# Performance work log

Hardware: AMD Instinct MI355X
Metric: run time of the kernel (lower is better)

## Reference

```python
import jax, jax.numpy as jnp
import numpy as np

B, N, DIM_IN, DIM_OUT, EMBED, CHEB_K = 32, 2000, 64, 64, 16, 3


def setup_inputs() -> dict:
    key = jax.random.key(0)
    ks = jax.random.split(key, 6)
    return {
        "x": jax.random.normal(ks[0], (B, N, DIM_IN), dtype=jnp.float32),
        "node_embeddings": jax.random.normal(ks[1], (N, EMBED), dtype=jnp.float32),
        "nodevec1": jax.random.normal(ks[2], (N, EMBED), dtype=jnp.float32),
        "nodevec2": jax.random.normal(ks[3], (EMBED, N), dtype=jnp.float32),
        "weights_pool": jax.random.normal(ks[4], (EMBED, CHEB_K, DIM_IN, DIM_OUT), dtype=jnp.float32) * 0.1,
        "bias_pool": jax.random.normal(ks[5], (EMBED, DIM_OUT), dtype=jnp.float32) * 0.1,
    }


def reference(x, node_embeddings, nodevec1, nodevec2, weights_pool, bias_pool):
    n = node_embeddings.shape[0]
    # adaptive adjacency: softmax(relu(nodevec1 @ nodevec2)) over rows' neighbors
    s = jax.nn.softmax(jax.nn.relu(nodevec1 @ nodevec2), axis=1)  # [N, N]
    # Chebyshev polynomial stack: T0 = I, T1 = S, Tk = 2 S Tk-1 - Tk-2
    support_set = [jnp.eye(n, dtype=x.dtype), s]
    for _ in range(2, CHEB_K):
        support_set.append(2.0 * s @ support_set[-1] - support_set[-2])
    supports = jnp.stack(support_set, axis=0)  # [K, N, N]
    # node-conditioned weights / bias
    weights = jnp.einsum('nd,dkio->nkio', node_embeddings, weights_pool)  # [N, K, I, O]
    bias = node_embeddings @ bias_pool  # [N, O]
    # graph conv: aggregate then per-node combine
    x_g = jnp.einsum('knm,bmc->bnkc', supports, x)  # [B, N, K, I]
    out = jnp.einsum('bnki,nkio->bno', x_g, weights) + bias  # [B, N, O]
    return out
```

## Files before the change

### kernel.cpp

```cpp
#include <hip/hip_runtime.h>

#define N_NODES 2000
#define NP      2048
#define KB      63
#define KB3     66
#define BATCH   32
#define DIM     64
#define EMB     16
#define KI      192
#define WCOLS   12288

typedef __bf16 bf16;
typedef __attribute__((ext_vector_type(8))) __bf16 bf16x8;
typedef __attribute__((ext_vector_type(4))) float  f32x4;

struct alignas(8) bf16x4pk { bf16 v[4]; };


#define Z0   (WCOLS * 32)
#define Z1   (Z0 + N_NODES * 32)
#define Z2   (Z1 + 3 * NP * 32)
#define PREP_SM_BLK   2554
#define PREP_BLOCKS   (N_NODES + 1024 + PREP_SM_BLK)

#define PW_BLOCKS 1200

__global__ __launch_bounds__(256) void prep_fused(
    const float* __restrict__ nv1, const float* __restrict__ nv2,
    bf16* __restrict__ Sp,
    const float* __restrict__ X, bf16* __restrict__ Xtp, bf16* __restrict__ Xbf,
    const float* __restrict__ wp, const float* __restrict__ emb,
    bf16* __restrict__ wpT2, bf16* __restrict__ embp, bf16* __restrict__ Sp63)
{
    const int bid = blockIdx.x;
    const int tid = threadIdx.x;

    if (bid < N_NODES) {
        const int row = bid;
        const int j0  = tid * 8;
        __shared__ float sa[EMB];
        __shared__ float wred[4];
        __shared__ float bcast;
        if (tid < EMB) sa[tid] = nv1[row * EMB + tid];
        __syncthreads();

        const bool active = (tid < 250);
        float v[8] = {0,0,0,0,0,0,0,0};
        if (active) {
#pragma unroll
            for (int d = 0; d < EMB; ++d) {
                const float sd = sa[d];
                const float4 q0 = *(const float4*)&nv2[d * N_NODES + j0];
                const float4 q1 = *(const float4*)&nv2[d * N_NODES + j0 + 4];
                v[0] += sd * q0.x; v[1] += sd * q0.y; v[2] += sd * q0.z; v[3] += sd * q0.w;
                v[4] += sd * q1.x; v[5] += sd * q1.y; v[6] += sd * q1.z; v[7] += sd * q1.w;
            }
        }
        float lmax = 0.0f;
#pragma unroll
        for (int jj = 0; jj < 8; ++jj) { v[jj] = fmaxf(v[jj], 0.0f); lmax = fmaxf(lmax, v[jj]); }
#pragma unroll
        for (int off = 32; off > 0; off >>= 1)
            lmax = fmaxf(lmax, __shfl_down(lmax, off, 64));
        if ((tid & 63) == 0) wred[tid >> 6] = lmax;
        __syncthreads();
        if (tid == 0) bcast = fmaxf(fmaxf(wred[0], wred[1]), fmaxf(wred[2], wred[3]));
        __syncthreads();
        const float rmax = bcast;

        float lsum = 0.0f;
        if (active) {
#pragma unroll
            for (int jj = 0; jj < 8; ++jj) { v[jj] = __expf(v[jj] - rmax); lsum += v[jj]; }
        }
#pragma unroll
        for (int off = 32; off > 0; off >>= 1)
            lsum += __shfl_down(lsum, off, 64);
        if ((tid & 63) == 0) wred[tid >> 6] = lsum;
        __syncthreads();
        if (tid == 0) bcast = wred[0] + wred[1] + wred[2] + wred[3];
        __syncthreads();
        const float inv = 1.0f / bcast;

        if (tid < 252) {
            bf16x8 pk;
#pragma unroll
            for (int jj = 0; jj < 8; ++jj)
                pk[jj] = (bf16)(active ? v[jj] * inv : 0.0f);
            const int kb = j0 >> 5, q = (j0 >> 3) & 3;
            const int nt = row >> 6, r = row & 63;
            *(bf16x8*)&Sp[((size_t)(kb * 32 + nt) * 256 + q * 64 + r) * 8] = pk;
        }
    } else if (bid < N_NODES + 1024) {
        const int t  = bid - N_NODES;
        const int b  = t >> 5;
        const int m0 = (t & 31) * 64;
        __shared__ bf16 T[64][72];
#pragma unroll
        for (int i = 0; i < 4; ++i) {
            int idx = i * 256 + tid;
            int r  = idx >> 4;
            int c4 = (idx & 15) * 4;
            int m  = m0 + r;
            float4 v = make_float4(0.f, 0.f, 0.f, 0.f);
            if (m < N_NODES)
                v = *(const float4*)&X[((size_t)b * N_NODES + m) * DIM + c4];
            bf16x4pk pk;
            pk.v[0] = (bf16)v.x; pk.v[1] = (bf16)v.y;
            pk.v[2] = (bf16)v.z; pk.v[3] = (bf16)v.w;
            if (m < N_NODES)
                *(bf16x4pk*)&Xbf[((size_t)b * N_NODES + m) * DIM + c4] = pk;
            T[c4 + 0][r] = pk.v[0];
            T[c4 + 1][r] = pk.v[1];
            T[c4 + 2][r] = pk.v[2];
            T[c4 + 3][r] = pk.v[3];
        }
        __syncthreads();
#pragma unroll
        for (int i = 0; i < 2; ++i) {
            int idx = i * 256 + tid;
            int c   = idx >> 3;
            int mch = idx & 7;
            int kb  = (m0 >> 5) + (mch >> 2);
            if (kb < KB) {
                int q = mch & 3;
                bf16x8 vv = *(const bf16x8*)&T[c][mch * 8];
                *(bf16x8*)&Xtp[((size_t)(b * KB3 + kb) * 256 + q * 64 + c) * 8] = vv;
            }
        }
    } else {
        int idx = (bid - N_NODES - 1024) * 256 + tid;
        if (idx < Z0) {
            int col = idx >> 5, d = idx & 31;
            int o  = col / KI;
            int kk = col - o * KI;
            int cheb = kk >> 6, i = kk & 63;
            float v = (d < EMB) ? wp[(((d * 3 + cheb) * 64 + i) * 64) + o] : 0.0f;
            wpT2[idx] = (bf16)v;
        } else if (idx < Z1) {
            int j = idx - Z0;
            int n = j >> 5, d = j & 31;
            float v = (d < EMB) ? emb[n * EMB + d] : 0.0f;
            embp[j] = (bf16)v;
        } else if (idx < Z2) {
            Sp63[idx - Z1] = (bf16)0.0f;
        }
    }
}

__global__ __launch_bounds__(256, 3) void spmm_reg(
    const bf16* __restrict__ Ap, const bf16* __restrict__ Btp,
    bf16* __restrict__ Ybf, bf16* __restrict__ Ytp,
    const bf16* __restrict__ embp, const bf16* __restrict__ wpT2,
    bf16* __restrict__ W, int write_ytp)
{
    const int bid  = blockIdx.x;
    const int tid  = threadIdx.x;
    const int lane = tid & 63, wave = tid >> 6;
    const int l15  = lane & 15, quad = lane >> 4;

    if (bid < 512) {
        const int kx = bid & 7, j = bid >> 3;
        const int ntB = (j & 7) + 8 * (kx & 1);
        const int b   = ((j >> 3) << 2) + (kx >> 1);
        const int n0  = ntB * 128;

        const bf16* aptr = Ap + ((size_t)(ntB * 2 + (wave >> 1)) * 256
                                 + quad * 64 + (wave & 1) * 32 + l15) * 8;
        const bf16* bptr = Btp + ((size_t)(b * KB3) * 256
                                  + quad * 64 + l15) * 8;

        f32x4 acc[2][4] = {};

        bf16x8 A0, A1, B0, B1, B2, B3;
        {
            A0 = *(const bf16x8*)(aptr);
            A1 = *(const bf16x8*)(aptr + 128);
            B0 = *(const bf16x8*)(bptr);
            B1 = *(const bf16x8*)(bptr + 128);
            B2 = *(const bf16x8*)(bptr + 256);
            B3 = *(const bf16x8*)(bptr + 384);
        }
#pragma unroll 2
        for (int s = 0; s < 66; ++s) {
            bf16x8 nA0, nA1, nB0, nB1, nB2, nB3;
            if (s + 1 < 66) {
                const bf16* pa = aptr + (size_t)(s + 1) * 65536;
                const bf16* pb = bptr + (size_t)(s + 1) * 2048;
                nA0 = *(const bf16x8*)(pa);
                nA1 = *(const bf16x8*)(pa + 128);
                nB0 = *(const bf16x8*)(pb);
                nB1 = *(const bf16x8*)(pb + 128);
                nB2 = *(const bf16x8*)(pb + 256);
                nB3 = *(const bf16x8*)(pb + 384);
            }
            acc[0][0] = __builtin_amdgcn_mfma_f32_16x16x32_bf16(A0, B0, acc[0][0], 0, 0, 0);
            acc[0][1] = __builtin_amdgcn_mfma_f32_16x16x32_bf16(A0, B1, acc[0][1], 0, 0, 0);
            acc[0][2] = __builtin_amdgcn_mfma_f32_16x16x32_bf16(A0, B2, acc[0][2], 0, 0, 0);
            acc[0][3] = __builtin_amdgcn_mfma_f32_16x16x32_bf16(A0, B3, acc[0][3], 0, 0, 0);
            acc[1][0] = __builtin_amdgcn_mfma_f32_16x16x32_bf16(A1, B0, acc[1][0], 0, 0, 0);
            acc[1][1] = __builtin_amdgcn_mfma_f32_16x16x32_bf16(A1, B1, acc[1][1], 0, 0, 0);
            acc[1][2] = __builtin_amdgcn_mfma_f32_16x16x32_bf16(A1, B2, acc[1][2], 0, 0, 0);
            acc[1][3] = __builtin_amdgcn_mfma_f32_16x16x32_bf16(A1, B3, acc[1][3], 0, 0, 0);
            A0 = nA0; A1 = nA1;
            B0 = nB0; B1 = nB1; B2 = nB2; B3 = nB3;
        }

#pragma unroll
        for (int rt = 0; rt < 2; ++rt) {
            const int nbase = n0 + (wave >> 1) * 64 + (wave & 1) * 32
                              + rt * 16 + quad * 4;
#pragma unroll
            for (int ct = 0; ct < 4; ++ct) {
                const int c = ct * 16 + l15;
#pragma unroll
                for (int r = 0; r < 4; ++r) {
                    int n = nbase + r;
                    if (n < N_NODES)
                        Ybf[((size_t)b * N_NODES + n) * DIM + c] = (bf16)acc[rt][ct][r];
                }
                if (write_ytp && nbase + 4 <= N_NODES) {
                    const int kb2 = nbase >> 5;
                    const int kq  = (nbase & 31) >> 3;
                    const int j4  = nbase & 7;
                    bf16x4pk pk;
                    pk.v[0] = (bf16)acc[rt][ct][0];
                    pk.v[1] = (bf16)acc[rt][ct][1];
                    pk.v[2] = (bf16)acc[rt][ct][2];
                    pk.v[3] = (bf16)acc[rt][ct][3];
                    *(bf16x4pk*)&Ytp[((size_t)(b * KB3 + kb2) * 256 + kq * 64 + c) * 8 + j4] = pk;
                }
            }
        }
    } else {
        __shared__ bf16 Cs[16][264];

        const int pid     = bid - 512;
        const int colbase = (pid % 48) * 256;
        const int ng0     = (pid / 48) * 5;

        bf16x8 bfr[4];
#pragma unroll
        for (int ct = 0; ct < 4; ++ct) {
            const int col = colbase + wave * 64 + ct * 16 + l15;
            bfr[ct] = *(const bf16x8*)&wpT2[(size_t)col * 32 + quad * 8];
        }
        bf16x8 afs[5];
#pragma unroll
        for (int g = 0; g < 5; ++g)
            afs[g] = *(const bf16x8*)&embp[(size_t)((ng0 + g) * 16 + l15) * 32 + quad * 8];
        const f32x4 zero = {};

#pragma unroll
        for (int g = 0; g < 5; ++g) {
            const int n0 = (ng0 + g) * 16;
#pragma unroll
            for (int ct = 0; ct < 4; ++ct) {
                f32x4 acc = __builtin_amdgcn_mfma_f32_16x16x32_bf16(afs[g], bfr[ct], zero, 0, 0, 0);
#pragma unroll
                for (int r = 0; r < 4; ++r)
                    Cs[quad * 4 + r][wave * 64 + ct * 16 + l15] = (bf16)acc[r];
            }
            __syncthreads();
            {
                const int row = tid >> 4;
                const int c16 = (tid & 15) * 16;
                bf16x8 v0 = *(const bf16x8*)&Cs[row][c16];
                bf16x8 v1 = *(const bf16x8*)&Cs[row][c16 + 8];
                bf16* dst = &W[(size_t)(n0 + row) * WCOLS + colbase + c16];
                *(bf16x8*)dst       = v0;
                *(bf16x8*)(dst + 8) = v1;
            }
            __syncthreads();
        }
    }
}

__global__ __launch_bounds__(256) void combine_node(
    const bf16* __restrict__ xbf, const bf16* __restrict__ y1bf,
    const bf16* __restrict__ y2bf, const float* __restrict__ emb,
    const float* __restrict__ bp, const bf16* __restrict__ W,
    float* __restrict__ out)
{
    const int n   = blockIdx.x;
    const int tid = threadIdx.x;
    const int lane = tid & 63, wave = tid >> 6;
    const int l15 = lane & 15, quad = lane >> 4;

    __shared__ bf16 As[BATCH][200];
    __shared__ bf16 Ws[DIM][200];
    __shared__ float bias_s[DIM];
    __shared__ float emb_s[EMB];

    if (tid < EMB) emb_s[tid] = emb[n * EMB + tid];

    {
        const int b  = tid >> 3;
        const int c8 = (tid & 7) * 8;
        const size_t base = ((size_t)b * N_NODES + n) * DIM + c8;
        bf16x8 vx = *(const bf16x8*)&xbf [base];
        bf16x8 v1 = *(const bf16x8*)&y1bf[base];
        bf16x8 v2 = *(const bf16x8*)&y2bf[base];
        bf16x8 p2;
#pragma unroll
        for (int e = 0; e < 8; ++e)
            p2[e] = (bf16)(2.0f * (float)v2[e] - (float)vx[e]);
        *(bf16x8*)&As[b][c8]       = vx;
        *(bf16x8*)&As[b][64 + c8]  = v1;
        *(bf16x8*)&As[b][128 + c8] = p2;
    }
    {
        const bf16* Wn = W + (size_t)n * WCOLS;
#pragma unroll
        for (int jj = 0; jj < 6; ++jj) {
            int chunk = jj * 256 + tid;
            int o  = chunk / 24;
            int kc = chunk - o * 24;
            bf16x8 v = *(const bf16x8*)&Wn[(size_t)chunk * 8];
            *(bf16x8*)&Ws[o][kc * 8] = v;
        }
    }
    __syncthreads();

    if (tid < DIM) {
        float s = 0.0f;
#pragma unroll
        for (int d = 0; d < EMB; ++d) s += emb_s[d] * bp[d * DIM + tid];
        bias_s[tid] = s;
    }

    bf16x8 af[2][6];
#pragma unroll
    for (int mt = 0; mt < 2; ++mt)
#pragma unroll
        for (int ks = 0; ks < 6; ++ks)
            af[mt][ks] = *(const bf16x8*)&As[mt * 16 + l15][ks * 32 + quad * 8];

    f32x4 acc[2] = {};
#pragma unroll
    for (int ks = 0; ks < 6; ++ks) {
        bf16x8 bfr = *(const bf16x8*)&Ws[wave * 16 + l15][ks * 32 + quad * 8];
        acc[0] = __builtin_amdgcn_mfma_f32_16x16x32_bf16(af[0][ks], bfr, acc[0], 0, 0, 0);
        acc[1] = __builtin_amdgcn_mfma_f32_16x16x32_bf16(af[1][ks], bfr, acc[1], 0, 0, 0);
    }
    __syncthreads();

    const int o = wave * 16 + l15;
    const float bv = bias_s[o];
#pragma unroll
    for (int mt = 0; mt < 2; ++mt)
#pragma unroll
        for (int r = 0; r < 4; ++r) {
            int b = mt * 16 + quad * 4 + r;
            out[((size_t)b * N_NODES + n) * DIM + o] = acc[mt][r] + bv;
        }
}

extern "C" void kernel_launch(void* const* d_in, const int* in_sizes, int n_in,
                              void* d_out, int out_size, void* d_ws, size_t ws_size,
                              hipStream_t stream) {
    const float* x   = (const float*)d_in[0];
    const float* emb = (const float*)d_in[1];
    const float* nv1 = (const float*)d_in[2];
    const float* nv2 = (const float*)d_in[3];
    const float* wp  = (const float*)d_in[4];
    const float* bp  = (const float*)d_in[5];
    float* out = (float*)d_out;

    char* w = (char*)d_ws;
    bf16* Sp   = (bf16*)w;  w += (size_t)KB3 * NP * 32 * 2;
    bf16* xTp  = (bf16*)w;  w += (size_t)BATCH * KB3 * DIM * 32 * 2;
    bf16* y1Tp = (bf16*)w;  w += (size_t)BATCH * KB3 * DIM * 32 * 2;
    bf16* xbf  = (bf16*)w;  w += (size_t)BATCH * N_NODES * DIM * 2;
    bf16* y1bf = (bf16*)w;  w += (size_t)BATCH * N_NODES * DIM * 2;
    bf16* y2bf = (bf16*)w;  w += (size_t)BATCH * N_NODES * DIM * 2;
    bf16* wpT2 = (bf16*)w;  w += (size_t)WCOLS * 32 * 2;
    bf16* embp = (bf16*)w;  w += (size_t)N_NODES * 32 * 2;
    bf16* W    = (bf16*)w;

    prep_fused<<<PREP_BLOCKS, 256, 0, stream>>>(
        nv1, nv2, Sp, x, xTp, xbf, wp, emb, wpT2, embp,
        Sp + (size_t)63 * NP * 32);
    spmm_reg<<<512 + PW_BLOCKS, 256, 0, stream>>>(Sp, xTp, y1bf, y1Tp, embp, wpT2, W, 1);
    spmm_reg<<<512, 256, 0, stream>>>(Sp, y1Tp, y2bf, y1Tp, embp, wpT2, W, 0);
    combine_node<<<N_NODES, 256, 0, stream>>>(xbf, y1bf, y2bf, emb, bp, W, out);
}
```

Before: 172.7 us.

## Split the SpMM K loop across two wave groups with an LDS reduction

The SpMM kernel moves to 512-thread blocks. Two groups of four waves each handle half of the 66 K-steps for the same output tile, and the partial accumulators are summed through shared memory before the epilogue writes the result. The aim is to shorten the serial dependent MFMA/load chain per block and put more waves on each CU to hide latency. The weight-generation branch packs two former work units per 512-thread block so the total work stays the same. The cost is an extra LDS round trip, a barrier, and higher per-block register and LDS pressure, which could lower occupancy.

```diff
diff --git a/kernel.cpp b/kernel.cpp
--- a/kernel.cpp
+++ b/kernel.cpp
@@ -23,7 +23,7 @@
 #define PREP_SM_BLK   2554
 #define PREP_BLOCKS   (N_NODES + 1024 + PREP_SM_BLK)
 
-#define PW_BLOCKS 1200
+#define PW_BLOCKS 600
 
 __global__ __launch_bounds__(256) void prep_fused(
     const float* __restrict__ nv1, const float* __restrict__ nv2,
@@ -148,43 +148,48 @@
     }
 }
 
-__global__ __launch_bounds__(256, 3) void spmm_reg(
+__global__ __launch_bounds__(512, 4) void spmm_ks(
     const bf16* __restrict__ Ap, const bf16* __restrict__ Btp,
     bf16* __restrict__ Ybf, bf16* __restrict__ Ytp,
     const bf16* __restrict__ embp, const bf16* __restrict__ wpT2,
     bf16* __restrict__ W, int write_ytp)
 {
+    __shared__ __align__(16) char smem[32768];
     const int bid  = blockIdx.x;
     const int tid  = threadIdx.x;
-    const int lane = tid & 63, wave = tid >> 6;
-    const int l15  = lane & 15, quad = lane >> 4;
+    const int lane = tid & 63;
+    const int l15  = lane & 15, quad = (lane >> 4) & 3;
 
     if (bid < 512) {
+        const int wave = tid >> 6;
+        const int kh   = wave >> 2;
+        const int w4   = wave & 3;
+
         const int kx = bid & 7, j = bid >> 3;
         const int ntB = (j & 7) + 8 * (kx & 1);
         const int b   = ((j >> 3) << 2) + (kx >> 1);
         const int n0  = ntB * 128;
 
-        const bf16* aptr = Ap + ((size_t)(ntB * 2 + (wave >> 1)) * 256
-                                 + quad * 64 + (wave & 1) * 32 + l15) * 8;
+        const bf16* aptr = Ap + ((size_t)(ntB * 2 + (w4 >> 1)) * 256
+                                 + quad * 64 + (w4 & 1) * 32 + l15) * 8
+                              + (size_t)(kh * 33) * 65536;
         const bf16* bptr = Btp + ((size_t)(b * KB3) * 256
-                                  + quad * 64 + l15) * 8;
+                                  + quad * 64 + l15) * 8
+                               + (size_t)(kh * 33) * 2048;
 
         f32x4 acc[2][4] = {};
 
         bf16x8 A0, A1, B0, B1, B2, B3;
-        {
-            A0 = *(const bf16x8*)(aptr);
-            A1 = *(const bf16x8*)(aptr + 128);
-            B0 = *(const bf16x8*)(bptr);
-            B1 = *(const bf16x8*)(bptr + 128);
-            B2 = *(const bf16x8*)(bptr + 256);
-            B3 = *(const bf16x8*)(bptr + 384);
-        }
+        A0 = *(const bf16x8*)(aptr);
+        A1 = *(const bf16x8*)(aptr + 128);
+        B0 = *(const bf16x8*)(bptr);
+        B1 = *(const bf16x8*)(bptr + 128);
+        B2 = *(const bf16x8*)(bptr + 256);
+        B3 = *(const bf16x8*)(bptr + 384);
 #pragma unroll 2
-        for (int s = 0; s < 66; ++s) {
+        for (int s = 0; s < 33; ++s) {
             bf16x8 nA0, nA1, nB0, nB1, nB2, nB3;
-            if (s + 1 < 66) {
+            if (s + 1 < 33) {
                 const bf16* pa = aptr + (size_t)(s + 1) * 65536;
                 const bf16* pb = bptr + (size_t)(s + 1) * 2048;
                 nA0 = *(const bf16x8*)(pa);
@@ -206,43 +211,70 @@
             B0 = nB0; B1 = nB1; B2 = nB2; B3 = nB3;
         }
 
-#pragma unroll
-        for (int rt = 0; rt < 2; ++rt) {
-            const int nbase = n0 + (wave >> 1) * 64 + (wave & 1) * 32
-                              + rt * 16 + quad * 4;
-#pragma unroll
-            for (int ct = 0; ct < 4; ++ct) {
-                const int c = ct * 16 + l15;
-#pragma unroll
-                for (int r = 0; r < 4; ++r) {
-                    int n = nbase + r;
-                    if (n < N_NODES)
-                        Ybf[((size_t)b * N_NODES + n) * DIM + c] = (bf16)acc[rt][ct][r];
+        float* red = (float*)smem;
+        if (kh == 1) {
+#pragma unroll
+            for (int rt = 0; rt < 2; ++rt)
+#pragma unroll
+                for (int ct = 0; ct < 4; ++ct)
+#pragma unroll
+                    for (int r = 0; r < 4; ++r)
+                        red[((rt * 4 + ct) * 4 + r) * 256 + w4 * 64 + lane]
+                            = acc[rt][ct][r];
+        }
+        __syncthreads();
+        if (kh == 0) {
+#pragma unroll
+            for (int rt = 0; rt < 2; ++rt)
+#pragma unroll
+                for (int ct = 0; ct < 4; ++ct)
+#pragma unroll
+                    for (int r = 0; r < 4; ++r)
+                        acc[rt][ct][r] +=
+                            red[((rt * 4 + ct) * 4 + r) * 256 + w4 * 64 + lane];
+
+#pragma unroll
+            for (int rt = 0; rt < 2; ++rt) {
+                const int nbase = n0 + (w4 >> 1) * 64 + (w4 & 1) * 32
+                                  + rt * 16 + quad * 4;
+#pragma unroll
+                for (int ct = 0; ct < 4; ++ct) {
+                    const int c = ct * 16 + l15;
+#pragma unroll
+                    for (int r = 0; r < 4; ++r) {
+                        int n = nbase + r;
+                        if (n < N_NODES)
+                            Ybf[((size_t)b * N_NODES + n) * DIM + c] = (bf16)acc[rt][ct][r];
+                    }
+                    if (write_ytp && nbase + 4 <= N_NODES) {
+                        const int kb2 = nbase >> 5;
+                        const int kq  = (nbase & 31) >> 3;
+                        const int j4  = nbase & 7;
+                        bf16x4pk pk;
+                        pk.v[0] = (bf16)acc[rt][ct][0];
+                        pk.v[1] = (bf16)acc[rt][ct][1];
+                        pk.v[2] = (bf16)acc[rt][ct][2];
+                        pk.v[3] = (bf16)acc[rt][ct][3];
+                        *(bf16x4pk*)&Ytp[((size_t)(b * KB3 + kb2) * 256 + kq * 64 + c) * 8 + j4] = pk;
+                    }
                 }
-                if (write_ytp && nbase + 4 <= N_NODES) {
-                    const int kb2 = nbase >> 5;
-                    const int kq  = (nbase & 31) >> 3;
-                    const int j4  = nbase & 7;
-                    bf16x4pk pk;
-                    pk.v[0] = (bf16)acc[rt][ct][0];
-                    pk.v[1] = (bf16)acc[rt][ct][1];
-                    pk.v[2] = (bf16)acc[rt][ct][2];
-                    pk.v[3] = (bf16)acc[rt][ct][3];
-                    *(bf16x4pk*)&Ytp[((size_t)(b * KB3 + kb2) * 256 + kq * 64 + c) * 8 + j4] = pk;
-                }
             }
         }
     } else {
-        __shared__ bf16 Cs[16][264];
-
-        const int pid     = bid - 512;
-        const int colbase = (pid % 48) * 256;
-        const int ng0     = (pid / 48) * 5;
+        bf16 (*Cs)[16][264] = (bf16(*)[16][264])smem;
+
+        const int half = tid >> 8;
+        const int t2   = tid & 255;
+        const int w2   = t2 >> 6;
+
+        const int unit    = (bid - 512) * 2 + half;
+        const int colbase = (unit % 48) * 256;
+        const int ng0     = (unit / 48) * 5;
 
         bf16x8 bfr[4];
 #pragma unroll
         for (int ct = 0; ct < 4; ++ct) {
-            const int col = colbase + wave * 64 + ct * 16 + l15;
+            const int col = colbase + w2 * 64 + ct * 16 + l15;
             bfr[ct] = *(const bf16x8*)&wpT2[(size_t)col * 32 + quad * 8];
         }
         bf16x8 afs[5];
@@ -259,14 +291,14 @@
                 f32x4 acc = __builtin_amdgcn_mfma_f32_16x16x32_bf16(afs[g], bfr[ct], zero, 0, 0, 0);
 #pragma unroll
                 for (int r = 0; r < 4; ++r)
-                    Cs[quad * 4 + r][wave * 64 + ct * 16 + l15] = (bf16)acc[r];
+                    Cs[half][quad * 4 + r][w2 * 64 + ct * 16 + l15] = (bf16)acc[r];
             }
             __syncthreads();
             {
-                const int row = tid >> 4;
-                const int c16 = (tid & 15) * 16;
-                bf16x8 v0 = *(const bf16x8*)&Cs[row][c16];
-                bf16x8 v1 = *(const bf16x8*)&Cs[row][c16 + 8];
+                const int row = t2 >> 4;
+                const int c16 = (t2 & 15) * 16;
+                bf16x8 v0 = *(const bf16x8*)&Cs[half][row][c16];
+                bf16x8 v1 = *(const bf16x8*)&Cs[half][row][c16 + 8];
                 bf16* dst = &W[(size_t)(n0 + row) * WCOLS + colbase + c16];
                 *(bf16x8*)dst       = v0;
                 *(bf16x8*)(dst + 8) = v1;
@@ -381,7 +413,7 @@
     prep_fused<<<PREP_BLOCKS, 256, 0, stream>>>(
         nv1, nv2, Sp, x, xTp, xbf, wp, emb, wpT2, embp,
         Sp + (size_t)63 * NP * 32);
-    spmm_reg<<<512 + PW_BLOCKS, 256, 0, stream>>>(Sp, xTp, y1bf, y1Tp, embp, wpT2, W, 1);
-    spmm_reg<<<512, 256, 0, stream>>>(Sp, y1Tp, y2bf, y1Tp, embp, wpT2, W, 0);
+    spmm_ks<<<512 + PW_BLOCKS, 512, 0, stream>>>(Sp, xTp, y1bf, y1Tp, embp, wpT2, W, 1);
+    spmm_ks<<<512, 512, 0, stream>>>(Sp, y1Tp, y2bf, y1Tp, embp, wpT2, W, 0);
     combine_node<<<N_NODES, 256, 0, stream>>>(xbf, y1bf, y2bf, emb, bp, W, out);
 }
```

New measurement: 176.2 us. No clear change (+2.0%).
